# Kernel optimization log

Measured on AMD Instinct MI355X. Metric: run time of the kernel, lower is better.

The kernel has to match this reference:

```python
import jax, jax.numpy as jnp
from jax import lax
import numpy as np

B, T, H = 131072, 49, 8  # batch, seq_len, hidden_size


def lstm_layer(x_tbi, W_ih, W_hh, b_ih, b_hh):
    """Single PyTorch-convention LSTM layer. x_tbi: [T, B, in]. Returns hs: [T, B, H]."""
    Tn, Bn = x_tbi.shape[0], x_tbi.shape[1]
    Hn = W_hh.shape[1]
    # Precompute input contributions for all timesteps: [T, B, 4H]
    xg = jnp.einsum('tbi,gi->tbg', x_tbi, W_ih) + b_ih + b_hh

    def step(carry, xt):
        h, c = carry
        g = xt + h @ W_hh.T                      # [B, 4H]
        i, f, gg, o = jnp.split(g, 4, axis=-1)   # PyTorch gate order: i, f, g, o
        i = jax.nn.sigmoid(i)
        f = jax.nn.sigmoid(f)
        gg = jnp.tanh(gg)
        o = jax.nn.sigmoid(o)
        c = f * c + i * gg
        h = o * jnp.tanh(c)
        return (h, c), h

    h0 = jnp.zeros((Bn, Hn), x_tbi.dtype)
    (_, _), hs = lax.scan(step, (h0, h0), xg)
    return hs


def setup_inputs() -> dict:
    key = jax.random.key(0)
    ks = jax.random.split(key, 11)
    s1 = 1.0 / np.sqrt(H)  # PyTorch uniform(-1/sqrt(H), 1/sqrt(H)) init
    u = lambda k, shape: jax.random.uniform(k, shape, jnp.float32, -s1, s1)
    return {
        'X': jax.random.normal(ks[0], (B, T, 1), jnp.float32),
        'W_ih0': u(ks[1], (4 * H, 1)),
        'W_hh0': u(ks[2], (4 * H, H)),
        'b_ih0': u(ks[3], (4 * H,)),
        'b_hh0': u(ks[4], (4 * H,)),
        'W_ih1': u(ks[5], (4 * H, H)),
        'W_hh1': u(ks[6], (4 * H, H)),
        'b_ih1': u(ks[7], (4 * H,)),
        'b_hh1': u(ks[8], (4 * H,)),
        'W_lin': u(ks[9], (1, H)),
        'b_lin': u(ks[10], (1,)),
    }


def reference(X, W_ih0, W_hh0, b_ih0, b_hh0, W_ih1, W_hh1, b_ih1, b_hh1, W_lin, b_lin):
    x = jnp.swapaxes(X, 0, 1)                     # [T, B, 1]
    h1 = lstm_layer(x, W_ih0, W_hh0, b_ih0, b_hh0)  # [T, B, H]
    h2 = lstm_layer(h1, W_ih1, W_hh1, b_ih1, b_hh1)  # [T, B, H]
    # relu -> linear -> relu -> take last timestep -> squeeze.
    # Slicing commutes with the pointwise/linear ops, so compute only on last step.
    hlast = jax.nn.relu(h2[-1])                   # [B, H]
    y = jax.nn.relu(hlast @ W_lin.T + b_lin)      # [B, 1]
    return y[:, 0]                                # [B]
```

## Files before the change

kernel.cpp:

```cpp
#include <hip/hip_runtime.h>

#define SWZ(v, imm) __int_as_float(__builtin_amdgcn_ds_swizzle(__float_as_int(v), (imm)))
#define BCAST(v, k) SWZ(v, (((k) << 5) | 0x18))
#define BCAST8(dst, v)                                                         \
    dst[0] = BCAST(v, 0); dst[1] = BCAST(v, 1); dst[2] = BCAST(v, 2);          \
    dst[3] = BCAST(v, 3); dst[4] = BCAST(v, 4); dst[5] = BCAST(v, 5);          \
    dst[6] = BCAST(v, 6); dst[7] = BCAST(v, 7);
#define RXOR(v, m) SWZ(v, (((m) << 10) | 0x1F))

__device__ __forceinline__ float fast_sig(float x) {
    float e = __builtin_amdgcn_exp2f(-1.44269504088896340736f * x);
    return __builtin_amdgcn_rcpf(1.0f + e);
}
__device__ __forceinline__ float fast_tanh(float x) {
    float e = __builtin_amdgcn_exp2f(2.88539008177792681472f * x);
    return 1.0f - 2.0f * __builtin_amdgcn_rcpf(e + 1.0f);
}

constexpr int T_STEPS = 49;

__global__ __launch_bounds__(256) void lstm2_kernel(
    const float* __restrict__ X,
    const float* __restrict__ W_ih0, const float* __restrict__ W_hh0,
    const float* __restrict__ b_ih0, const float* __restrict__ b_hh0,
    const float* __restrict__ W_ih1, const float* __restrict__ W_hh1,
    const float* __restrict__ b_ih1, const float* __restrict__ b_hh1,
    const float* __restrict__ W_lin, const float* __restrict__ b_lin,
    float* __restrict__ out, int Bn)
{
    const int tid = blockIdx.x * 256 + threadIdx.x;
    const int b   = tid >> 3;
    const int j   = threadIdx.x & 7;

    if (b >= Bn) return;

    float wx0[4], bb0[4], bb1[4];
    float whh0[4][8], wi1[4][8], whh1[4][8];
#pragma unroll
    for (int g = 0; g < 4; ++g) {
        const int r = g * 8 + j;
        wx0[g] = W_ih0[r];
        bb0[g] = b_ih0[r] + b_hh0[r];
        bb1[g] = b_ih1[r] + b_hh1[r];
#pragma unroll
        for (int k = 0; k < 8; ++k) {
            whh0[g][k] = W_hh0[r * 8 + k];
            wi1[g][k]  = W_ih1[r * 8 + k];
            whh1[g][k] = W_hh1[r * 8 + k];
        }
    }
    const float wlin = W_lin[j];
    const float blin = b_lin[0];

    float h1 = 0.f, c1 = 0.f, h2 = 0.f, c2 = 0.f;
    float h1b[8], h2b[8];
#pragma unroll
    for (int k = 0; k < 8; ++k) { h1b[k] = 0.f; h2b[k] = 0.f; }

    const float* xp = X + (long long)b * T_STEPS;

#pragma unroll 1
    for (int t = 0; t < T_STEPS; ++t) {
        const float x = xp[t];

        float a[4];
#pragma unroll
        for (int g = 0; g < 4; ++g) {
            a[g] = fmaf(x, wx0[g], bb0[g]);
#pragma unroll
            for (int k = 0; k < 8; ++k) a[g] = fmaf(whh0[g][k], h1b[k], a[g]);
        }
        float gi = fast_sig(a[0]);
        float gf = fast_sig(a[1]);
        float gg = fast_tanh(a[2]);
        float go = fast_sig(a[3]);
        c1 = fmaf(gf, c1, gi * gg);
        h1 = go * fast_tanh(c1);

        BCAST8(h1b, h1);
        BCAST8(h2b, h2);

        float a2[4];
#pragma unroll
        for (int g = 0; g < 4; ++g) {
            a2[g] = bb1[g];
#pragma unroll
            for (int k = 0; k < 8; ++k) a2[g] = fmaf(wi1[g][k], h1b[k], a2[g]);
#pragma unroll
            for (int k = 0; k < 8; ++k) a2[g] = fmaf(whh1[g][k], h2b[k], a2[g]);
        }
        gi = fast_sig(a2[0]);
        gf = fast_sig(a2[1]);
        gg = fast_tanh(a2[2]);
        go = fast_sig(a2[3]);
        c2 = fmaf(gf, c2, gi * gg);
        h2 = go * fast_tanh(c2);
    }

    float v = fmaxf(h2, 0.f) * wlin;
    v += RXOR(v, 1);
    v += RXOR(v, 2);
    v += RXOR(v, 4);
    if (j == 0) out[b] = fmaxf(v + blin, 0.f);
}

extern "C" void kernel_launch(void* const* d_in, const int* in_sizes, int n_in,
                              void* d_out, int out_size, void* d_ws, size_t ws_size,
                              hipStream_t stream) {
    const float* X     = (const float*)d_in[0];
    const float* W_ih0 = (const float*)d_in[1];
    const float* W_hh0 = (const float*)d_in[2];
    const float* b_ih0 = (const float*)d_in[3];
    const float* b_hh0 = (const float*)d_in[4];
    const float* W_ih1 = (const float*)d_in[5];
    const float* W_hh1 = (const float*)d_in[6];
    const float* b_ih1 = (const float*)d_in[7];
    const float* b_hh1 = (const float*)d_in[8];
    const float* W_lin = (const float*)d_in[9];
    const float* b_lin = (const float*)d_in[10];
    float* out = (float*)d_out;

    const int Bn = in_sizes[0] / T_STEPS;
    const int threads = Bn * 8;
    const int block = 256;
    const int grid = (threads + block - 1) / block;

    lstm2_kernel<<<grid, block, 0, stream>>>(X, W_ih0, W_hh0, b_ih0, b_hh0,
                                             W_ih1, W_hh1, b_ih1, b_hh1,
                                             W_lin, b_lin, out, Bn);
}
```

Baseline: 214.7 us.

## Process two batch rows per thread with packed fp32 FMA instructions

Each 8-lane group now handles two batch elements, and the gate matmuls and elementwise math use v_pk_fma_f32/v_pk_mul/v_pk_add through inline asm with op_sel to broadcast a weight half. The aim is to halve the VALU instruction count per element and amortise the weight registers across two sequences. In exchange the per-thread register footprint and swizzle count per thread double, the grid halves, launch bounds request 2 waves per EU, and odd batch sizes are no longer handled.

```diff
diff --git a/kernel.cpp b/kernel.cpp
--- a/kernel.cpp
+++ b/kernel.cpp
@@ -1,107 +1,170 @@
 #include <hip/hip_runtime.h>
+
+typedef float f2 __attribute__((ext_vector_type(2)));
 
 #define SWZ(v, imm) __int_as_float(__builtin_amdgcn_ds_swizzle(__float_as_int(v), (imm)))
 #define BCAST(v, k) SWZ(v, (((k) << 5) | 0x18))
-#define BCAST8(dst, v)                                                         \
-    dst[0] = BCAST(v, 0); dst[1] = BCAST(v, 1); dst[2] = BCAST(v, 2);          \
-    dst[3] = BCAST(v, 3); dst[4] = BCAST(v, 4); dst[5] = BCAST(v, 5);          \
-    dst[6] = BCAST(v, 6); dst[7] = BCAST(v, 7);
 #define RXOR(v, m) SWZ(v, (((m) << 10) | 0x1F))
 
-__device__ __forceinline__ float fast_sig(float x) {
-    float e = __builtin_amdgcn_exp2f(-1.44269504088896340736f * x);
-    return __builtin_amdgcn_rcpf(1.0f + e);
+__device__ __forceinline__ f2 pk_fma(f2 a, f2 b, f2 c) {
+    f2 d; asm("v_pk_fma_f32 %0, %1, %2, %3" : "=v"(d) : "v"(a), "v"(b), "v"(c)); return d;
 }
-__device__ __forceinline__ float fast_tanh(float x) {
-    float e = __builtin_amdgcn_exp2f(2.88539008177792681472f * x);
-    return 1.0f - 2.0f * __builtin_amdgcn_rcpf(e + 1.0f);
+__device__ __forceinline__ f2 pk_fma_lo(f2 w, f2 h, f2 c) {
+    f2 d; asm("v_pk_fma_f32 %0, %1, %2, %3 op_sel:[0,0,0] op_sel_hi:[0,1,1]"
+              : "=v"(d) : "v"(w), "v"(h), "v"(c)); return d;
+}
+__device__ __forceinline__ f2 pk_fma_hi(f2 w, f2 h, f2 c) {
+    f2 d; asm("v_pk_fma_f32 %0, %1, %2, %3 op_sel:[1,0,0] op_sel_hi:[1,1,1]"
+              : "=v"(d) : "v"(w), "v"(h), "v"(c)); return d;
+}
+__device__ __forceinline__ f2 pk_mul(f2 a, f2 b) {
+    f2 d; asm("v_pk_mul_f32 %0, %1, %2" : "=v"(d) : "v"(a), "v"(b)); return d;
+}
+__device__ __forceinline__ f2 pk_add(f2 a, f2 b) {
+    f2 d; asm("v_pk_add_f32 %0, %1, %2" : "=v"(d) : "v"(a), "v"(b)); return d;
+}
+
+__device__ __forceinline__ f2 sig2(f2 x) {
+    const f2 nl2e = { -1.44269504088896340736f, -1.44269504088896340736f };
+    const f2 one2 = { 1.0f, 1.0f };
+    f2 m = pk_mul(x, nl2e);
+    f2 e; e.x = __builtin_amdgcn_exp2f(m.x); e.y = __builtin_amdgcn_exp2f(m.y);
+    f2 s = pk_add(e, one2);
+    f2 r; r.x = __builtin_amdgcn_rcpf(s.x); r.y = __builtin_amdgcn_rcpf(s.y);
+    return r;
+}
+__device__ __forceinline__ f2 tanh2(f2 x) {
+    const f2 p2l2e = { 2.88539008177792681472f, 2.88539008177792681472f };
+    const f2 one2  = { 1.0f, 1.0f };
+    const f2 neg22 = { -2.0f, -2.0f };
+    f2 m = pk_mul(x, p2l2e);
+    f2 e; e.x = __builtin_amdgcn_exp2f(m.x); e.y = __builtin_amdgcn_exp2f(m.y);
+    f2 s = pk_add(e, one2);
+    f2 r; r.x = __builtin_amdgcn_rcpf(s.x); r.y = __builtin_amdgcn_rcpf(s.y);
+    return pk_fma(r, neg22, one2);
 }
 
 constexpr int T_STEPS = 49;
 
-__global__ __launch_bounds__(256) void lstm2_kernel(
+__global__ __launch_bounds__(256, 2) void lstm2_kernel(
     const float* __restrict__ X,
     const float* __restrict__ W_ih0, const float* __restrict__ W_hh0,
     const float* __restrict__ b_ih0, const float* __restrict__ b_hh0,
     const float* __restrict__ W_ih1, const float* __restrict__ W_hh1,
     const float* __restrict__ b_ih1, const float* __restrict__ b_hh1,
     const float* __restrict__ W_lin, const float* __restrict__ b_lin,
-    float* __restrict__ out, int Bn)
+    float* __restrict__ out, int nq)
 {
     const int tid = blockIdx.x * 256 + threadIdx.x;
-    const int b   = tid >> 3;
+    const int q   = tid >> 3;
     const int j   = threadIdx.x & 7;
+    if (q >= nq) return;
 
-    if (b >= Bn) return;
-
-    float wx0[4], bb0[4], bb1[4];
-    float whh0[4][8], wi1[4][8], whh1[4][8];
+    f2 whh0p[4][4], wi1p[4][4], whh1p[4][4];
+    f2 bb0d[4], bb1d[4];
 #pragma unroll
     for (int g = 0; g < 4; ++g) {
         const int r = g * 8 + j;
-        wx0[g] = W_ih0[r];
-        bb0[g] = b_ih0[r] + b_hh0[r];
-        bb1[g] = b_ih1[r] + b_hh1[r];
+        const f2* w0 = (const f2*)(W_hh0 + r * 8);
+        const f2* w1 = (const f2*)(W_ih1 + r * 8);
+        const f2* w2 = (const f2*)(W_hh1 + r * 8);
 #pragma unroll
-        for (int k = 0; k < 8; ++k) {
-            whh0[g][k] = W_hh0[r * 8 + k];
-            wi1[g][k]  = W_ih1[r * 8 + k];
-            whh1[g][k] = W_hh1[r * 8 + k];
+        for (int kp = 0; kp < 4; ++kp) {
+            whh0p[g][kp] = w0[kp];
+            wi1p[g][kp]  = w1[kp];
+            whh1p[g][kp] = w2[kp];
         }
+        float b0 = b_ih0[r] + b_hh0[r];  bb0d[g].x = b0; bb0d[g].y = b0;
+        float b1 = b_ih1[r] + b_hh1[r];  bb1d[g].x = b1; bb1d[g].y = b1;
     }
+    f2 wx0p0, wx0p1;
+    wx0p0.x = W_ih0[0 * 8 + j];  wx0p0.y = W_ih0[1 * 8 + j];
+    wx0p1.x = W_ih0[2 * 8 + j];  wx0p1.y = W_ih0[3 * 8 + j];
     const float wlin = W_lin[j];
     const float blin = b_lin[0];
 
-    float h1 = 0.f, c1 = 0.f, h2 = 0.f, c2 = 0.f;
-    float h1b[8], h2b[8];
+    f2 h1, c1, h2, c2;
+    h1 = 0.f; c1 = 0.f; h2 = 0.f; c2 = 0.f;
+    f2 h1b[8], h2b[8];
 #pragma unroll
     for (int k = 0; k < 8; ++k) { h1b[k] = 0.f; h2b[k] = 0.f; }
 
-    const float* xp = X + (long long)b * T_STEPS;
+    const float* xp0 = X + (long long)(2 * q) * T_STEPS;
+    const float* xp1 = xp0 + T_STEPS;
 
 #pragma unroll 1
     for (int t = 0; t < T_STEPS; ++t) {
-        const float x = xp[t];
+        f2 x2; x2.x = xp0[t]; x2.y = xp1[t];
 
-        float a[4];
+        f2 a[4];
+        a[0] = pk_fma_lo(wx0p0, x2, bb0d[0]);
+        a[1] = pk_fma_hi(wx0p0, x2, bb0d[1]);
+        a[2] = pk_fma_lo(wx0p1, x2, bb0d[2]);
+        a[3] = pk_fma_hi(wx0p1, x2, bb0d[3]);
 #pragma unroll
         for (int g = 0; g < 4; ++g) {
-            a[g] = fmaf(x, wx0[g], bb0[g]);
 #pragma unroll
-            for (int k = 0; k < 8; ++k) a[g] = fmaf(whh0[g][k], h1b[k], a[g]);
+            for (int kp = 0; kp < 4; ++kp) {
+                a[g] = pk_fma_lo(whh0p[g][kp], h1b[2 * kp],     a[g]);
+                a[g] = pk_fma_hi(whh0p[g][kp], h1b[2 * kp + 1], a[g]);
+            }
         }
-        float gi = fast_sig(a[0]);
-        float gf = fast_sig(a[1]);
-        float gg = fast_tanh(a[2]);
-        float go = fast_sig(a[3]);
-        c1 = fmaf(gf, c1, gi * gg);
-        h1 = go * fast_tanh(c1);
+        f2 gi = sig2(a[0]);
+        f2 gf = sig2(a[1]);
+        f2 gg = tanh2(a[2]);
+        f2 go = sig2(a[3]);
+        c1 = pk_fma(gf, c1, pk_mul(gi, gg));
+        h1 = pk_mul(go, tanh2(c1));
 
-        BCAST8(h1b, h1);
-        BCAST8(h2b, h2);
+        h1b[0].x = BCAST(h1.x, 0); h1b[0].y = BCAST(h1.y, 0);
+        h1b[1].x = BCAST(h1.x, 1); h1b[1].y = BCAST(h1.y, 1);
+        h1b[2].x = BCAST(h1.x, 2); h1b[2].y = BCAST(h1.y, 2);
+        h1b[3].x = BCAST(h1.x, 3); h1b[3].y = BCAST(h1.y, 3);
+        h1b[4].x = BCAST(h1.x, 4); h1b[4].y = BCAST(h1.y, 4);
+        h1b[5].x = BCAST(h1.x, 5); h1b[5].y = BCAST(h1.y, 5);
+        h1b[6].x = BCAST(h1.x, 6); h1b[6].y = BCAST(h1.y, 6);
+        h1b[7].x = BCAST(h1.x, 7); h1b[7].y = BCAST(h1.y, 7);
+        h2b[0].x = BCAST(h2.x, 0); h2b[0].y = BCAST(h2.y, 0);
+        h2b[1].x = BCAST(h2.x, 1); h2b[1].y = BCAST(h2.y, 1);
+        h2b[2].x = BCAST(h2.x, 2); h2b[2].y = BCAST(h2.y, 2);
+        h2b[3].x = BCAST(h2.x, 3); h2b[3].y = BCAST(h2.y, 3);
+        h2b[4].x = BCAST(h2.x, 4); h2b[4].y = BCAST(h2.y, 4);
+        h2b[5].x = BCAST(h2.x, 5); h2b[5].y = BCAST(h2.y, 5);
+        h2b[6].x = BCAST(h2.x, 6); h2b[6].y = BCAST(h2.y, 6);
+        h2b[7].x = BCAST(h2.x, 7); h2b[7].y = BCAST(h2.y, 7);
 
-        float a2[4];
+        f2 a2[4];
 #pragma unroll
         for (int g = 0; g < 4; ++g) {
-            a2[g] = bb1[g];
+            a2[g] = bb1d[g];
 #pragma unroll
-            for (int k = 0; k < 8; ++k) a2[g] = fmaf(wi1[g][k], h1b[k], a2[g]);
+            for (int kp = 0; kp < 4; ++kp) {
+                a2[g] = pk_fma_lo(wi1p[g][kp], h1b[2 * kp],     a2[g]);
+                a2[g] = pk_fma_hi(wi1p[g][kp], h1b[2 * kp + 1], a2[g]);
+            }
 #pragma unroll
-            for (int k = 0; k < 8; ++k) a2[g] = fmaf(whh1[g][k], h2b[k], a2[g]);
+            for (int kp = 0; kp < 4; ++kp) {
+                a2[g] = pk_fma_lo(whh1p[g][kp], h2b[2 * kp],     a2[g]);
+                a2[g] = pk_fma_hi(whh1p[g][kp], h2b[2 * kp + 1], a2[g]);
+            }
         }
-        gi = fast_sig(a2[0]);
-        gf = fast_sig(a2[1]);
-        gg = fast_tanh(a2[2]);
-        go = fast_sig(a2[3]);
-        c2 = fmaf(gf, c2, gi * gg);
-        h2 = go * fast_tanh(c2);
+        gi = sig2(a2[0]);
+        gf = sig2(a2[1]);
+        gg = tanh2(a2[2]);
+        go = sig2(a2[3]);
+        c2 = pk_fma(gf, c2, pk_mul(gi, gg));
+        h2 = pk_mul(go, tanh2(c2));
     }
 
-    float v = fmaxf(h2, 0.f) * wlin;
-    v += RXOR(v, 1);
-    v += RXOR(v, 2);
-    v += RXOR(v, 4);
-    if (j == 0) out[b] = fmaxf(v + blin, 0.f);
+    float vx = fmaxf(h2.x, 0.f) * wlin;
+    float vy = fmaxf(h2.y, 0.f) * wlin;
+    vx += RXOR(vx, 1); vy += RXOR(vy, 1);
+    vx += RXOR(vx, 2); vy += RXOR(vy, 2);
+    vx += RXOR(vx, 4); vy += RXOR(vy, 4);
+    if (j == 0) {
+        f2 o; o.x = fmaxf(vx + blin, 0.f); o.y = fmaxf(vy + blin, 0.f);
+        *(f2*)(out + 2 * (long long)q) = o;
+    }
 }
 
 extern "C" void kernel_launch(void* const* d_in, const int* in_sizes, int n_in,
@@ -121,11 +184,12 @@
     float* out = (float*)d_out;
 
     const int Bn = in_sizes[0] / T_STEPS;
-    const int threads = Bn * 8;
+    const int nq = Bn >> 1;
+    const int threads = nq * 8;
     const int block = 256;
     const int grid = (threads + block - 1) / block;
 
     lstm2_kernel<<<grid, block, 0, stream>>>(X, W_ih0, W_hh0, b_ih0, b_hh0,
                                              W_ih1, W_hh1, b_ih1, b_hh1,
-                                             W_lin, b_lin, out, Bn);
+                                             W_lin, b_lin, out, nq);
 }
```

New measurement: 193.9 us. 9.7% less time.
